# Performance work log

Measured on AMD Instinct MI355X. Metric: run time of the kernel, lower is better.

Reference implementation:

```python
import jax, jax.numpy as jnp
import numpy as np

LAYERS, BLOCKS = 10, 4
RES_CH, END_CH, CLASSES, GROUPS = 32, 256, 256, 1
BN_EPS = 1e-5


def conv1x1(x, w, b):
    # x: (bn, Cin, L), w: (Cout, Cin), b: (Cout,)
    return jnp.einsum('oc,bcl->bol', w, x) + b[None, :, None]


def mish(x):
    return x * jnp.tanh(jax.nn.softplus(x))


def concat_mish(x):
    return mish(jnp.concatenate((x, -x), axis=1))


def channel_shuffle(x, groups):
    if groups == 1:
        return x
    bn, c, l = x.shape
    return x.reshape(bn, groups, c // groups, l).transpose(0, 2, 1, 3).reshape(bn, c, l)


def batchnorm_train(x, g, b):
    # BatchNorm1d in training mode: per-channel stats over (batch, length), biased var
    m = jnp.mean(x, axis=(0, 2), keepdims=True)
    v = jnp.mean((x - m) ** 2, axis=(0, 2), keepdims=True)
    return (x - m) * jax.lax.rsqrt(v + BN_EPS) * g[None, :, None] + b[None, :, None]


def dilate(x, dilation, init_dilation, pad_start=True):
    bn, c, l = x.shape
    if dilation == 1:
        x = jnp.transpose(x, (1, 2, 0)).reshape(c, l * init_dilation, bn // init_dilation)
        return jnp.transpose(x, (2, 0, 1))
    f = dilation // init_dilation
    if f == 1:
        return x
    new_l = (l + f - 1) // f * f
    if new_l != l:
        pad = (new_l - l, 0) if pad_start else (0, new_l - l)
        x = jnp.pad(x, ((0, 0), (0, 0), pad))
        l = new_l
    l //= f
    bn *= f
    x = jnp.transpose(x, (1, 2, 0)).reshape(c, l, bn)
    return jnp.transpose(x, (2, 0, 1))


def setup_inputs() -> dict:
    key = jax.random.key(0)
    ks = iter(jax.random.split(key, 32))
    nl = LAYERS * BLOCKS
    f32 = jnp.float32
    inp = {
        'x': jax.random.normal(next(ks), (8, CLASSES, 8192), dtype=f32),
        'start_w': jax.random.normal(next(ks), (RES_CH, CLASSES), dtype=f32) * 0.05,
        'start_b': jnp.zeros((RES_CH,), f32),
        'gate_w': jax.random.normal(next(ks), (nl, RES_CH // 2, RES_CH), dtype=f32) * 0.15,
        'gate_b': jnp.zeros((nl, RES_CH // 2), f32),
        'res_w': jax.random.normal(next(ks), (nl, RES_CH, RES_CH), dtype=f32) * 0.15,
        'res_b': jnp.zeros((nl, RES_CH), f32),
        'bn_g': jnp.ones((nl, RES_CH), f32),
        'bn_b': jnp.zeros((nl, RES_CH), f32),
        'end_bn1_g': jnp.ones((RES_CH,), f32),
        'end_bn1_b': jnp.zeros((RES_CH,), f32),
        'end_conv1_w': jax.random.normal(next(ks), (END_CH // 2, 2 * RES_CH), dtype=f32) * 0.1,
        'end_conv1_b': jnp.zeros((END_CH // 2,), f32),
        'end_bn2_g': jnp.ones((END_CH // 2,), f32),
        'end_bn2_b': jnp.zeros((END_CH // 2,), f32),
        'end_conv2_w': jax.random.normal(next(ks), (CLASSES, END_CH), dtype=f32) * 0.05,
        'end_conv2_b': jnp.zeros((CLASSES,), f32),
    }
    return inp


def reference(x, start_w, start_b, gate_w, gate_b, res_w, res_b, bn_g, bn_b,
              end_bn1_g, end_bn1_b, end_conv1_w, end_conv1_b,
              end_bn2_g, end_bn2_b, end_conv2_w, end_conv2_b):
    x = conv1x1(x, start_w, start_b)
    prev_dilation = 1
    i = 0
    for block in range(BLOCKS):
        for layer in range(LAYERS):
            x = dilate(x, 2 ** layer, prev_dilation)
            prev_dilation = 2 ** layer
            x0 = x
            h = concat_mish(conv1x1(x, gate_w[i], gate_b[i]))
            h = channel_shuffle(h, GROUPS)
            h = batchnorm_train(conv1x1(h, res_w[i], res_b[i]), bn_g[i], bn_b[i])
            h = channel_shuffle(h, GROUPS)
            x = x0 + h
            i += 1
    x = concat_mish(batchnorm_train(x, end_bn1_g, end_bn1_b))
    x = concat_mish(batchnorm_train(conv1x1(x, end_conv1_w, end_conv1_b), end_bn2_g, end_bn2_b))
    x = conv1x1(x, end_conv2_w, end_conv2_b)
    x = dilate(x, 1, 2 ** (LAYERS - 1))
    return x
```

## Files before the change

kernel.cpp:

```cpp
#include <hip/hip_runtime.h>

#define BS 256
#define BSP 512
#define NBLKP 128
#define NBLK 256
#define STATS_F   0
#define W2T_F     46080
#define XBUF_F    131072
#define RBUF_F    2228224
#define WS_NEED_BYTES (4325376ull * 4ull)
#define CNTS_U  4096

__device__ __forceinline__ void mish2(float v, float& mp, float& mn) {
  float vc = fminf(fmaxf(v, -30.f), 30.f);
  float u  = __expf(vc);
  float n1 = u * (u + 2.f);
  mp = v * n1 * __builtin_amdgcn_rcpf(n1 + 2.f);
  float n2 = fmaf(2.f, u, 1.f);
  float d2 = fmaf(2.f * u, u, n2);
  mn = -v * n2 * __builtin_amdgcn_rcpf(d2);
}

__device__ __forceinline__ float coherent_ld(const float* p) {
  return __hip_atomic_load(p, __ATOMIC_RELAXED, __HIP_MEMORY_SCOPE_AGENT);
}
__device__ __forceinline__ void coherent_st(float* p, float v) {
  __hip_atomic_store(p, v, __ATOMIC_RELAXED, __HIP_MEMORY_SCOPE_AGENT);
}

template<int NT>
__device__ __forceinline__ void block_reduce_stats(const float (&vals)[32],
    float* s_red, float* s_p2, float* slot, int t) {
  #pragma unroll
  for (int cc = 0; cc < 8; ++cc) {
    float4 v = make_float4(vals[cc*4+0], vals[cc*4+1], vals[cc*4+2], vals[cc*4+3]);
    *(float4*)(&s_red[t*32 + ((cc ^ (t & 7)) << 2)]) = v;
  }
  __syncthreads();
  {
    int q = t & 63, grp = t >> 6, c = q & 31;
    bool issq = (q >= 32);
    float acc = 0.f;
    #pragma clang loop unroll_count(8)
    for (int rr = 0; rr < 64; ++rr) {
      int row = grp * 64 + rr;
      float v = s_red[row*32 + ((((c >> 2) ^ (row & 7)) << 2) | (c & 3))];
      acc = fmaf(v, issq ? v : 1.f, acc);
    }
    s_p2[t] = acc;
  }
  __syncthreads();
  if (t < 64) {
    float tot = 0.f;
    #pragma unroll
    for (int g = 0; g < NT/64; ++g) tot += s_p2[t + g*64];
    unsafeAtomicAdd(&slot[(blockIdx.x & 15) * 64 + t], tot);
  }
  __syncthreads();
}

__device__ __forceinline__ void bn32_from_slot(const float* slot, const float* g,
    const float* b, float* sA, float* sB, float* s_tmp, int t) {
  if (t < 64) {
    float s = 0.f;
    #pragma unroll
    for (int rep = 0; rep < 16; ++rep) s += slot[rep*64 + t];
    s_tmp[t] = s;
  }
  __syncthreads();
  if (t < 32) {
    float mean = s_tmp[t] * (1.f/65536.f);
    float var  = fmaf(-mean, mean, s_tmp[t+32] * (1.f/65536.f));
    float sc   = g[t] * rsqrtf(var + 1e-5f);
    sA[t] = sc;
    sB[t] = fmaf(-mean, sc, b[t]);
  }
  __syncthreads();
}

__device__ __forceinline__ void bn32_slot_coh(const float* slot, const float* g,
    const float* b, float* sA, float* sB, float* s_tmp, int t) {
  if (t < 64) {
    float s = 0.f;
    #pragma unroll
    for (int rep = 0; rep < 16; ++rep) s += coherent_ld(&slot[rep*64 + t]);
    s_tmp[t] = s;
  }
  __syncthreads();
  if (t < 32) {
    float mean = s_tmp[t] * (1.f/65536.f);
    float var  = fmaf(-mean, mean, s_tmp[t+32] * (1.f/65536.f));
    float sc   = g[t] * rsqrtf(var + 1e-5f);
    sA[t] = sc;
    sB[t] = fmaf(-mean, sc, b[t]);
  }
  __syncthreads();
}

__device__ __forceinline__ void layer_convs(const float (&x)[32], float (&r)[32],
    const float* gw, const float* gb, const float* rw, const float* rb, int i) {
  float g[16];
  #pragma unroll
  for (int j = 0; j < 16; ++j) g[j] = gb[i*16 + j];
  #pragma unroll
  for (int j = 0; j < 16; ++j)
    #pragma unroll
    for (int k = 0; k < 32; ++k)
      g[j] = fmaf(gw[i*512 + j*32 + k], x[k], g[j]);
  float cm[32];
  #pragma unroll
  for (int j = 0; j < 16; ++j) mish2(g[j], cm[j], cm[j+16]);
  #pragma unroll
  for (int j = 0; j < 32; ++j) r[j] = rb[i*32 + j];
  #pragma unroll
  for (int j = 0; j < 32; ++j)
    #pragma unroll
    for (int k = 0; k < 32; ++k)
      r[j] = fmaf(rw[i*1024 + j*32 + k], cm[k], r[j]);
}

__device__ __forceinline__ void grid_sync_lean(float* base, unsigned gen) {
  __syncthreads();
  unsigned* cnts = (unsigned*)base + CNTS_U;
  if (threadIdx.x == 0) {
    __hip_atomic_fetch_add(&cnts[(blockIdx.x & 31) * 16], 1u,
                           __ATOMIC_RELAXED, __HIP_MEMORY_SCOPE_AGENT);
    unsigned sum;
    do {
      __builtin_amdgcn_s_sleep(1);
      sum = 0;
      #pragma unroll
      for (int x = 0; x < 32; ++x)
        sum += __hip_atomic_load(&cnts[x*16], __ATOMIC_RELAXED, __HIP_MEMORY_SCOPE_AGENT);
    } while (sum < gen * NBLKP);
  }
  __syncthreads();
}

__device__ __forceinline__ void grid_sync_p(float* base, unsigned gen, bool flush) {
  __syncthreads();
  unsigned* flags = (unsigned*)base;
  unsigned* cnts  = (unsigned*)base + CNTS_U;
  if (blockIdx.x == 0) {
    if (threadIdx.x == 0) {
      if (flush) __threadfence();
      __hip_atomic_fetch_add(&cnts[0], 1u, __ATOMIC_RELAXED, __HIP_MEMORY_SCOPE_AGENT);
      unsigned sum;
      do {
        __builtin_amdgcn_s_sleep(2);
        sum = 0;
        #pragma unroll
        for (int x = 0; x < 32; ++x)
          sum += __hip_atomic_load(&cnts[x*16], __ATOMIC_RELAXED, __HIP_MEMORY_SCOPE_AGENT);
      } while (sum < gen * NBLK);
    }
    __syncthreads();
    __hip_atomic_store(&flags[threadIdx.x * 16], gen,
                       __ATOMIC_RELAXED, __HIP_MEMORY_SCOPE_AGENT);
  } else {
    if (threadIdx.x == 0) {
      if (flush) __threadfence();
      __hip_atomic_fetch_add(&cnts[(blockIdx.x & 31) * 16], 1u,
                             __ATOMIC_RELAXED, __HIP_MEMORY_SCOPE_AGENT);
      while (__hip_atomic_load(&flags[blockIdx.x * 16],
                               __ATOMIC_RELAXED, __HIP_MEMORY_SCOPE_AGENT) < gen)
        __builtin_amdgcn_s_sleep(2);
    }
    __syncthreads();
  }
}

extern "C" __global__ void __launch_bounds__(BSP, 1)
qnet_p(const float* __restrict__ xin, const float* __restrict__ sw,
       const float* __restrict__ sb, const float* __restrict__ gw,
       const float* __restrict__ gb, const float* __restrict__ rw,
       const float* __restrict__ rb, const float* __restrict__ bng,
       const float* __restrict__ bnb, const float* __restrict__ e1g,
       const float* __restrict__ e1b, const float* __restrict__ c1w,
       const float* __restrict__ c1b, const float* __restrict__ c2w,
       float* __restrict__ ws)
{
  __shared__ float s_red[BSP*32];
  __shared__ float s_p2[BSP];
  __shared__ float s_A[32], s_B[32], s_tmp[64];
  const int t = threadIdx.x, p = blockIdx.x * BSP + t;
  float* stats = ws + STATS_F;
  float* w2t   = ws + W2T_F;
  float* xb    = ws + XBUF_F;
  float* syncb = ws + RBUF_F;
  unsigned gen = 0;
  { int o = p & 255, kk = p >> 8; w2t[kk*256 + o] = c2w[o*256 + kk]; }
  const int bb = p >> 13, ll = p & 8191;
  const int pbase = bb * 2097152 + ll;
  float x[32];
  #pragma unroll
  for (int j = 0; j < 32; ++j) x[j] = sb[j];
  #pragma clang loop unroll(disable)
  for (int c8 = 0; c8 < 32; ++c8) {
    float xv[8];
    #pragma unroll
    for (int cc = 0; cc < 8; ++cc) xv[cc] = xin[pbase + (c8*8+cc)*8192];
    #pragma unroll
    for (int j = 0; j < 32; ++j)
      #pragma unroll
      for (int cc = 0; cc < 8; ++cc)
        x[j] = fmaf(sw[j*256 + c8*8 + cc], xv[cc], x[j]);
  }
  float r[32];
  layer_convs(x, r, gw, gb, rw, rb, 0);
  block_reduce_stats<BSP>(r, s_red, s_p2, stats + 0, t);
  ++gen; grid_sync_lean(syncb, gen);
  #pragma clang loop unroll(disable)
  for (int i = 1; i < 40; ++i) {
    bn32_slot_coh(stats + (i-1)*1024, bng + (i-1)*32, bnb + (i-1)*32, s_A, s_B, s_tmp, t);
    #pragma unroll
    for (int c = 0; c < 32; ++c) x[c] += fmaf(r[c], s_A[c], s_B[c]);
    layer_convs(x, r, gw, gb, rw, rb, i);
    block_reduce_stats<BSP>(r, s_red, s_p2, stats + i*1024, t);
    ++gen; grid_sync_lean(syncb, gen);
  }
  bn32_slot_coh(stats + 39*1024, bng + 39*32, bnb + 39*32, s_A, s_B, s_tmp, t);
  #pragma unroll
  for (int c = 0; c < 32; ++c) {
    x[c] += fmaf(r[c], s_A[c], s_B[c]);
    xb[c*65536 + p] = x[c];
  }
  block_reduce_stats<BSP>(x, s_red, s_p2, stats + 40*1024, t);
  ++gen; grid_sync_lean(syncb, gen);
  bn32_slot_coh(stats + 40*1024, e1g, e1b, s_A, s_B, s_tmp, t);
  float mp[32], mn[32];
  #pragma unroll
  for (int c = 0; c < 32; ++c) {
    float xh = fmaf(x[c], s_A[c], s_B[c]);
    mish2(xh, mp[c], mn[c]);
  }
  #pragma clang loop unroll(disable)
  for (int pp = 0; pp < 4; ++pp) {
    float zc[32];
    #pragma unroll
    for (int j = 0; j < 32; ++j) zc[j] = c1b[pp*32 + j];
    #pragma unroll
    for (int j = 0; j < 32; ++j)
      #pragma unroll
      for (int k = 0; k < 32; ++k) {
        zc[j] = fmaf(c1w[(pp*32+j)*64 + k],      mp[k], zc[j]);
        zc[j] = fmaf(c1w[(pp*32+j)*64 + 32 + k], mn[k], zc[j]);
      }
    block_reduce_stats<BSP>(zc, s_red, s_p2, stats + (41+pp)*1024, t);
  }
}

__global__ void __launch_bounds__(BS, 2) k_end3(const float* __restrict__ e1g,
    const float* __restrict__ e1b, const float* __restrict__ c1w,
    const float* __restrict__ c1b, const float* __restrict__ e2g,
    const float* __restrict__ e2b, const float* __restrict__ c2b,
    float* __restrict__ out, float* __restrict__ ws) {
  __shared__ float s_A[32], s_B[32], s_tmp[64];
  __shared__ float s_A2[128], s_B2[128];
  __shared__ float s_ck[2048];
  __shared__ float4 wbuf4[512];
  __shared__ float s_c1b[128];
  __shared__ float s_c2b[32];
  int t = threadIdx.x;
  const int pA = blockIdx.x * 512 + t;
  const int pB = pA + 256;
  float* stats = ws + STATS_F; float* xb = ws + XBUF_F;
  const float* w2t = ws + W2T_F;
  const int ocb = blockIdx.y * 32;
  if (t < 32) ((float4*)s_c1b)[t] = ((const float4*)c1b)[t];
  else if (t < 40) ((float4*)s_c2b)[t-32] = ((const float4*)(c2b + ocb))[t-32];
  bn32_from_slot(stats + 40*1024, e1g, e1b, s_A, s_B, s_tmp, t);
  if (t < 128) {
    int pp = t >> 5, c = t & 31;
    const float* sl = stats + (41+pp)*1024;
    float S = 0.f, Q = 0.f;
    #pragma unroll
    for (int rep = 0; rep < 16; ++rep) { S += sl[rep*64 + c]; Q += sl[rep*64 + 32 + c]; }
    float mean = S * (1.f/65536.f);
    float var  = fmaf(-mean, mean, Q * (1.f/65536.f));
    float sc   = e2g[t] * rsqrtf(var + 1e-5f);
    s_A2[t] = sc;
    s_B2[t] = fmaf(-mean, sc, e2b[t]);
  }
  __syncthreads();
  float mpA[32], mnA[32], mpB[32], mnB[32];
  #pragma unroll
  for (int c = 0; c < 32; ++c) {
    float xhA = fmaf(xb[c*65536 + pA], s_A[c], s_B[c]);
    mish2(xhA, mpA[c], mnA[c]);
    float xhB = fmaf(xb[c*65536 + pB], s_A[c], s_B[c]);
    mish2(xhB, mpB[c], mnB[c]);
  }
  float acc[64];
  #pragma unroll
  for (int o = 0; o < 32; ++o) { acc[o] = s_c2b[o]; acc[32+o] = s_c2b[o]; }
  #pragma clang loop unroll(disable)
  for (int kc = 0; kc < 4; ++kc) {
    __syncthreads();
    { const float4* cs = (const float4*)(c1w + kc*2048);
      ((float4*)s_ck)[t]       = cs[t];
      ((float4*)s_ck)[256 + t] = cs[256 + t]; }
    #pragma unroll
    for (int q = 0; q < 2; ++q) {
      int f = q*256 + t;
      int r = f >> 3, o4 = f & 7;
      int kglob = (r < 32) ? (kc*32 + r) : (96 + kc*32 + r);
      wbuf4[f] = *((const float4*)(w2t + kglob*256 + ocb) + o4);
    }
    __syncthreads();
    #pragma clang loop unroll_count(2)
    for (int j = 0; j < 32; ++j) {
      const int k = kc*32 + j;
      float zA = s_c1b[k], zB = s_c1b[k];
      const float4* cw = (const float4*)&s_ck[j*64];
      #pragma unroll
      for (int k4 = 0; k4 < 8; ++k4) {
        float4 a = cw[k4], b = cw[8+k4];
        zA = fmaf(a.x, mpA[k4*4+0], zA);
        zA = fmaf(a.y, mpA[k4*4+1], zA);
        zA = fmaf(a.z, mpA[k4*4+2], zA);
        zA = fmaf(a.w, mpA[k4*4+3], zA);
        zA = fmaf(b.x, mnA[k4*4+0], zA);
        zA = fmaf(b.y, mnA[k4*4+1], zA);
        zA = fmaf(b.z, mnA[k4*4+2], zA);
        zA = fmaf(b.w, mnA[k4*4+3], zA);
        zB = fmaf(a.x, mpB[k4*4+0], zB);
        zB = fmaf(a.y, mpB[k4*4+1], zB);
        zB = fmaf(a.z, mpB[k4*4+2], zB);
        zB = fmaf(a.w, mpB[k4*4+3], zB);
        zB = fmaf(b.x, mnB[k4*4+0], zB);
        zB = fmaf(b.y, mnB[k4*4+1], zB);
        zB = fmaf(b.z, mnB[k4*4+2], zB);
        zB = fmaf(b.w, mnB[k4*4+3], zB);
      }
      float zhA = fmaf(zA, s_A2[k], s_B2[k]);
      float mpvA, mnvA; mish2(zhA, mpvA, mnvA);
      float zhB = fmaf(zB, s_A2[k], s_B2[k]);
      float mpvB, mnvB; mish2(zhB, mpvB, mnvB);
      const float4* w0 = &wbuf4[j*8];
      const float4* w1 = &wbuf4[(32 + j)*8];
      #pragma unroll
      for (int o4 = 0; o4 < 8; ++o4) {
        float4 a = w0[o4], b = w1[o4];
        acc[o4*4+0] = fmaf(a.x, mpvA, fmaf(b.x, mnvA, acc[o4*4+0]));
        acc[o4*4+1] = fmaf(a.y, mpvA, fmaf(b.y, mnvA, acc[o4*4+1]));
        acc[o4*4+2] = fmaf(a.z, mpvA, fmaf(b.z, mnvA, acc[o4*4+2]));
        acc[o4*4+3] = fmaf(a.w, mpvA, fmaf(b.w, mnvA, acc[o4*4+3]));
        acc[32+o4*4+0] = fmaf(a.x, mpvB, fmaf(b.x, mnvB, acc[32+o4*4+0]));
        acc[32+o4*4+1] = fmaf(a.y, mpvB, fmaf(b.y, mnvB, acc[32+o4*4+1]));
        acc[32+o4*4+2] = fmaf(a.z, mpvB, fmaf(b.z, mnvB, acc[32+o4*4+2]));
        acc[32+o4*4+3] = fmaf(a.w, mpvB, fmaf(b.w, mnvB, acc[32+o4*4+3]));
      }
    }
  }
  {
    int bbA = pA >> 13, llA = pA & 8191;
    int obA = bbA * 2097152 + ocb * 8192 + llA;
    #pragma unroll
    for (int o = 0; o < 32; ++o) out[obA + o*8192] = acc[o];
    int bbB = pB >> 13, llB = pB & 8191;
    int obB = bbB * 2097152 + ocb * 8192 + llB;
    #pragma unroll
    for (int o = 0; o < 32; ++o) out[obB + o*8192] = acc[32+o];
  }
}

#define W2T_FB  4608
#define STATS_OUT_OFF (8u*1024u*1024u)
#define SLOT_STRIDE 16384

__device__ __forceinline__ void grid_sync_fb(float* ws, unsigned gen, bool flush) {
  grid_sync_p(ws, gen, flush);
}
__device__ __forceinline__ void brs_fb(const float (&vals)[32],
    float* s_red, float* s_p2, float* slot, int t) {
  #pragma unroll
  for (int cc = 0; cc < 8; ++cc) {
    float4 v = make_float4(vals[cc*4+0], vals[cc*4+1], vals[cc*4+2], vals[cc*4+3]);
    *(float4*)(&s_red[t*32 + ((cc ^ (t & 7)) << 2)]) = v;
  }
  __syncthreads();
  {
    int q = t & 63, grp = t >> 6, c = q & 31;
    bool issq = (q >= 32);
    float acc = 0.f;
    #pragma clang loop unroll_count(8)
    for (int rr = 0; rr < 64; ++rr) {
      int row = grp * 64 + rr;
      float v = s_red[row*32 + ((((c >> 2) ^ (row & 7)) << 2) | (c & 3))];
      acc = fmaf(v, issq ? v : 1.f, acc);
    }
    s_p2[t] = acc;
  }
  __syncthreads();
  if (t < 64) {
    float tot = s_p2[t] + s_p2[t+64] + s_p2[t+128] + s_p2[t+192];
    coherent_st(&slot[blockIdx.x * 64 + t], tot);
  }
}

extern "C" __global__ void __launch_bounds__(BS, 1)
qnet_fb(const float* __restrict__ xin,
        const float* __restrict__ sw, const float* __restrict__ sb,
        const float* __restrict__ gw, const float* __restrict__ gb,
        const float* __restrict__ rw, const float* __restrict__ rb,
        const float* __restrict__ bng, const float* __restrict__ bnb,
        const float* __restrict__ e1g, const float* __restrict__ e1b,
        const float* __restrict__ c1w, const float* __restrict__ c1b,
        const float* __restrict__ e2g, const float* __restrict__ e2b,
        const float* __restrict__ c2w, const float* __restrict__ c2b,
        float* __restrict__ out, float* __restrict__ ws)
{
  __shared__ float s_red[BS*32];
  __shared__ float s_p2[BS];
  __shared__ float s_tot[64];
  __shared__ float s_bcA[128];
  __shared__ float s_bcB[128];
  const int t = threadIdx.x;
  const int p = blockIdx.x * BS + t;
  float* w2t = ws + W2T_FB;
  float* zg  = out;
  float* sg  = out + STATS_OUT_OFF;
  unsigned gen = 0;
  const int bb = p >> 13, ll = p & 8191;
  const int pbase = bb * 2097152 + ll;
  { int o = p & 255, kk = p >> 8; coherent_st(&w2t[kk*256 + o], c2w[o*256 + kk]); }
  float x[32];
  #pragma unroll
  for (int j = 0; j < 32; ++j) x[j] = sb[j];
  #pragma clang loop unroll(disable)
  for (int c8 = 0; c8 < 32; ++c8) {
    float xv[8];
    #pragma unroll
    for (int cc = 0; cc < 8; ++cc) xv[cc] = xin[pbase + (c8*8+cc)*8192];
    #pragma unroll
    for (int j = 0; j < 32; ++j)
      #pragma unroll
      for (int cc = 0; cc < 8; ++cc)
        x[j] = fmaf(sw[j*256 + c8*8 + cc], xv[cc], x[j]);
  }
  #pragma clang loop unroll(disable)
  for (int i = 0; i < 40; ++i) {
    float r[32];
    layer_convs(x, r, gw, gb, rw, rb, i);
    brs_fb(r, s_red, s_p2, sg + (size_t)i * SLOT_STRIDE, t);
    ++gen; grid_sync_fb(ws, gen, false);
    {
      int q = t & 63, w = t >> 6;
      const float* col = sg + (size_t)i * SLOT_STRIDE + q;
      float acc2 = 0.f;
      #pragma clang loop unroll_count(16)
      for (int j = 0; j < 64; ++j) acc2 += coherent_ld(&col[(w*64+j)*64]);
      s_p2[t] = acc2;
    }
    __syncthreads();
    if (t < 64) s_tot[t] = s_p2[t] + s_p2[t+64] + s_p2[t+128] + s_p2[t+192];
    __syncthreads();
    if (t < 32) {
      float mean = s_tot[t] * (1.f/65536.f);
      float var  = fmaf(-mean, mean, s_tot[t+32] * (1.f/65536.f));
      float sc   = bng[i*32+t] * rsqrtf(var + 1e-5f);
      s_bcA[t] = sc;
      s_bcB[t] = fmaf(-mean, sc, bnb[i*32+t]);
    }
    __syncthreads();
    #pragma unroll
    for (int c = 0; c < 32; ++c) x[c] += fmaf(r[c], s_bcA[c], s_bcB[c]);
  }
  brs_fb(x, s_red, s_p2, sg + 40 * SLOT_STRIDE, t);
  ++gen; grid_sync_fb(ws, gen, false);
  {
    int q = t & 63, w = t >> 6;
    const float* col = sg + (size_t)40 * SLOT_STRIDE + q;
    float acc2 = 0.f;
    #pragma clang loop unroll_count(16)
    for (int j = 0; j < 64; ++j) acc2 += coherent_ld(&col[(w*64+j)*64]);
    s_p2[t] = acc2;
  }
  __syncthreads();
  if (t < 64) s_tot[t] = s_p2[t] + s_p2[t+64] + s_p2[t+128] + s_p2[t+192];
  __syncthreads();
  if (t < 32) {
    float mean = s_tot[t] * (1.f/65536.f);
    float var  = fmaf(-mean, mean, s_tot[t+32] * (1.f/65536.f));
    float sc   = e1g[t] * rsqrtf(var + 1e-5f);
    s_bcA[t] = sc;
    s_bcB[t] = fmaf(-mean, sc, e1b[t]);
  }
  __syncthreads();
  float mp[32], mn[32];
  #pragma unroll
  for (int c = 0; c < 32; ++c) {
    float xh = fmaf(x[c], s_bcA[c], s_bcB[c]);
    mish2(xh, mp[c], mn[c]);
  }
  #pragma clang loop unroll(disable)
  for (int pp = 0; pp < 4; ++pp) {
    float zc[32];
    #pragma unroll
    for (int j = 0; j < 32; ++j) zc[j] = c1b[pp*32 + j];
    #pragma unroll
    for (int j = 0; j < 32; ++j)
      #pragma unroll
      for (int k = 0; k < 32; ++k) {
        zc[j] = fmaf(c1w[(pp*32+j)*64 + k],      mp[k], zc[j]);
        zc[j] = fmaf(c1w[(pp*32+j)*64 + 32 + k], mn[k], zc[j]);
      }
    #pragma unroll
    for (int j = 0; j < 32; ++j) zg[(pp*32+j)*65536 + p] = zc[j];
    brs_fb(zc, s_red, s_p2, sg + (size_t)(41+pp) * SLOT_STRIDE, t);
    __syncthreads();
  }
  ++gen; grid_sync_fb(ws, gen, false);
  {
    int slot = 41 + (t >> 6), q = t & 63;
    const float* col = sg + (size_t)slot * SLOT_STRIDE + q;
    float acc2 = 0.f;
    #pragma clang loop unroll_count(32)
    for (int b2 = 0; b2 < 256; ++b2) acc2 += coherent_ld(&col[b2*64]);
    s_p2[t] = acc2;
  }
  __syncthreads();
  if (t < 128) {
    float S = s_p2[((t>>5)<<6) | (t&31)];
    float Q = s_p2[((t>>5)<<6) | 32 | (t&31)];
    float mean = S * (1.f/65536.f);
    float var  = fmaf(-mean, mean, Q * (1.f/65536.f));
    float sc   = e2g[t] * rsqrtf(var + 1e-5f);
    s_bcA[t] = sc;
    s_bcB[t] = fmaf(-mean, sc, e2b[t]);
  }
  __syncthreads();
  float acc[256];
  #pragma unroll
  for (int o = 0; o < 256; ++o) acc[o] = c2b[o];
  float zv_next = zg[p];
  #pragma clang loop unroll(disable)
  for (int k = 0; k < 128; ++k) {
    float zv = zv_next;
    zv_next = zg[((k+1)&127)*65536 + p];
    float zh = fmaf(zv, s_bcA[k], s_bcB[k]);
    float mpv, mnv; mish2(zh, mpv, mnv);
    const float* w0 = &w2t[k*256];
    const float* w1 = &w2t[(k+128)*256];
    #pragma unroll
    for (int o = 0; o < 256; ++o)
      acc[o] = fmaf(w0[o], mpv, fmaf(w1[o], mnv, acc[o]));
  }
  ++gen; grid_sync_fb(ws, gen, true);
  #pragma unroll
  for (int o = 0; o < 256; ++o)
    out[bb*2097152 + o*8192 + ll] = acc[o];
}

extern "C" void kernel_launch(void* const* d_in, const int* in_sizes, int n_in,
                              void* d_out, int out_size, void* d_ws, size_t ws_size,
                              hipStream_t stream) {
  const float* xin = (const float*)d_in[0];
  const float* sw  = (const float*)d_in[1];
  const float* sb  = (const float*)d_in[2];
  const float* gw  = (const float*)d_in[3];
  const float* gb  = (const float*)d_in[4];
  const float* rw  = (const float*)d_in[5];
  const float* rb  = (const float*)d_in[6];
  const float* bng = (const float*)d_in[7];
  const float* bnb = (const float*)d_in[8];
  const float* e1g = (const float*)d_in[9];
  const float* e1b = (const float*)d_in[10];
  const float* c1w = (const float*)d_in[11];
  const float* c1b = (const float*)d_in[12];
  const float* e2g = (const float*)d_in[13];
  const float* e2b = (const float*)d_in[14];
  const float* c2w = (const float*)d_in[15];
  const float* c2b = (const float*)d_in[16];
  float* out = (float*)d_out;
  float* ws  = (float*)d_ws;

  if (ws_size >= WS_NEED_BYTES) {
    hipMemsetAsync(d_ws, 0, 45 * 1024 * 4, stream);
    hipMemsetAsync((char*)d_ws + (size_t)RBUF_F * 4, 0, 4608 * 4, stream);
    void* args[] = { &xin, &sw, &sb, &gw, &gb, &rw, &rb, &bng, &bnb,
                     &e1g, &e1b, &c1w, &c1b, &c2w, &ws };
    hipError_t err = hipLaunchCooperativeKernel((const void*)qnet_p,
                                                dim3(NBLKP), dim3(BSP), args, 0, stream);
    if (err != hipSuccess) {
      hipLaunchKernelGGL(qnet_p, dim3(NBLKP), dim3(BSP), 0, stream,
                         xin, sw, sb, gw, gb, rw, rb, bng, bnb,
                         e1g, e1b, c1w, c1b, c2w, ws);
    }
    k_end3<<<dim3(128, 8), BS, 0, stream>>>(e1g, e1b, c1w, c1b, e2g, e2b, c2b, out, ws);
  } else {
    hipMemsetAsync(d_ws, 0, (CNTS_U + 512) * 4, stream);
    void* args[] = { &xin, &sw, &sb, &gw, &gb, &rw, &rb, &bng, &bnb,
                     &e1g, &e1b, &c1w, &c1b, &e2g, &e2b, &c2w, &c2b, &out, &ws };
    hipError_t err = hipLaunchCooperativeKernel((const void*)qnet_fb,
                                                dim3(NBLK), dim3(BS), args, 0, stream);
    if (err != hipSuccess) {
      hipLaunchKernelGGL(qnet_fb, dim3(NBLK), dim3(BS), 0, stream,
                         xin, sw, sb, gw, gb, rw, rb, bng, bnb,
                         e1g, e1b, c1w, c1b, e2g, e2b, c2w, c2b, out, ws);
    }
  }
}
```

Before: 1.510 ms.

## Switch persistent kernel to 256 blocks of 256 threads and simplify end kernel

The cooperative main kernel now runs 256 blocks of 256 threads instead of 128 blocks of 512. The BN stat slots are widened to 64 replicas to spread atomic contention, and the workspace offsets are moved to match. The end kernel is restructured so each thread handles one position and 64 output channels. It reads the transposed end_conv2 weights straight from global memory instead of staging them in LDS. The trade is more blocks taking part in each grid barrier and more replicas to sum on every BN read, against less per-block LDS reduction work and lower register pressure.

```diff
diff --git a/kernel.cpp b/kernel.cpp
--- a/kernel.cpp
+++ b/kernel.cpp
@@ -1,13 +1,14 @@
 #include <hip/hip_runtime.h>
 
 #define BS 256
-#define BSP 512
-#define NBLKP 128
+#define NBLKP 256
 #define NBLK 256
+#define NREP 64
+#define SLOT_F 4096
 #define STATS_F   0
-#define W2T_F     46080
-#define XBUF_F    131072
-#define RBUF_F    2228224
+#define W2T_F     184320
+#define XBUF_F    262144
+#define SYNC_F    2359296
 #define WS_NEED_BYTES (4325376ull * 4ull)
 #define CNTS_U  4096
 
@@ -28,7 +29,6 @@
   __hip_atomic_store(p, v, __ATOMIC_RELAXED, __HIP_MEMORY_SCOPE_AGENT);
 }
 
-template<int NT>
 __device__ __forceinline__ void block_reduce_stats(const float (&vals)[32],
     float* s_red, float* s_p2, float* slot, int t) {
   #pragma unroll
@@ -51,10 +51,8 @@
   }
   __syncthreads();
   if (t < 64) {
-    float tot = 0.f;
-    #pragma unroll
-    for (int g = 0; g < NT/64; ++g) tot += s_p2[t + g*64];
-    unsafeAtomicAdd(&slot[(blockIdx.x & 15) * 64 + t], tot);
+    float tot = s_p2[t] + s_p2[t+64] + s_p2[t+128] + s_p2[t+192];
+    unsafeAtomicAdd(&slot[(blockIdx.x & (NREP-1)) * 64 + t], tot);
   }
   __syncthreads();
 }
@@ -64,7 +62,7 @@
   if (t < 64) {
     float s = 0.f;
     #pragma unroll
-    for (int rep = 0; rep < 16; ++rep) s += slot[rep*64 + t];
+    for (int rep = 0; rep < NREP; ++rep) s += slot[rep*64 + t];
     s_tmp[t] = s;
   }
   __syncthreads();
@@ -83,7 +81,7 @@
   if (t < 64) {
     float s = 0.f;
     #pragma unroll
-    for (int rep = 0; rep < 16; ++rep) s += coherent_ld(&slot[rep*64 + t]);
+    for (int rep = 0; rep < NREP; ++rep) s += coherent_ld(&slot[rep*64 + t]);
     s_tmp[t] = s;
   }
   __syncthreads();
@@ -170,7 +168,7 @@
   }
 }
 
-extern "C" __global__ void __launch_bounds__(BSP, 1)
+extern "C" __global__ void __launch_bounds__(BS, 1)
 qnet_p(const float* __restrict__ xin, const float* __restrict__ sw,
        const float* __restrict__ sb, const float* __restrict__ gw,
        const float* __restrict__ gb, const float* __restrict__ rw,
@@ -180,14 +178,14 @@
        const float* __restrict__ c1b, const float* __restrict__ c2w,
        float* __restrict__ ws)
 {
-  __shared__ float s_red[BSP*32];
-  __shared__ float s_p2[BSP];
+  __shared__ float s_red[BS*32];
+  __shared__ float s_p2[BS];
   __shared__ float s_A[32], s_B[32], s_tmp[64];
-  const int t = threadIdx.x, p = blockIdx.x * BSP + t;
+  const int t = threadIdx.x, p = blockIdx.x * BS + t;
   float* stats = ws + STATS_F;
   float* w2t   = ws + W2T_F;
   float* xb    = ws + XBUF_F;
-  float* syncb = ws + RBUF_F;
+  float* syncb = ws + SYNC_F;
   unsigned gen = 0;
   { int o = p & 255, kk = p >> 8; w2t[kk*256 + o] = c2w[o*256 + kk]; }
   const int bb = p >> 13, ll = p & 8191;
@@ -208,26 +206,26 @@
   }
   float r[32];
   layer_convs(x, r, gw, gb, rw, rb, 0);
-  block_reduce_stats<BSP>(r, s_red, s_p2, stats + 0, t);
+  block_reduce_stats(r, s_red, s_p2, stats + 0, t);
   ++gen; grid_sync_lean(syncb, gen);
   #pragma clang loop unroll(disable)
   for (int i = 1; i < 40; ++i) {
-    bn32_slot_coh(stats + (i-1)*1024, bng + (i-1)*32, bnb + (i-1)*32, s_A, s_B, s_tmp, t);
+    bn32_slot_coh(stats + (i-1)*SLOT_F, bng + (i-1)*32, bnb + (i-1)*32, s_A, s_B, s_tmp, t);
     #pragma unroll
     for (int c = 0; c < 32; ++c) x[c] += fmaf(r[c], s_A[c], s_B[c]);
     layer_convs(x, r, gw, gb, rw, rb, i);
-    block_reduce_stats<BSP>(r, s_red, s_p2, stats + i*1024, t);
+    block_reduce_stats(r, s_red, s_p2, stats + i*SLOT_F, t);
     ++gen; grid_sync_lean(syncb, gen);
   }
-  bn32_slot_coh(stats + 39*1024, bng + 39*32, bnb + 39*32, s_A, s_B, s_tmp, t);
+  bn32_slot_coh(stats + 39*SLOT_F, bng + 39*32, bnb + 39*32, s_A, s_B, s_tmp, t);
   #pragma unroll
   for (int c = 0; c < 32; ++c) {
     x[c] += fmaf(r[c], s_A[c], s_B[c]);
     xb[c*65536 + p] = x[c];
   }
-  block_reduce_stats<BSP>(x, s_red, s_p2, stats + 40*1024, t);
+  block_reduce_stats(x, s_red, s_p2, stats + 40*SLOT_F, t);
   ++gen; grid_sync_lean(syncb, gen);
-  bn32_slot_coh(stats + 40*1024, e1g, e1b, s_A, s_B, s_tmp, t);
+  bn32_slot_coh(stats + 40*SLOT_F, e1g, e1b, s_A, s_B, s_tmp, t);
   float mp[32], mn[32];
   #pragma unroll
   for (int c = 0; c < 32; ++c) {
@@ -246,11 +244,11 @@
         zc[j] = fmaf(c1w[(pp*32+j)*64 + k],      mp[k], zc[j]);
         zc[j] = fmaf(c1w[(pp*32+j)*64 + 32 + k], mn[k], zc[j]);
       }
-    block_reduce_stats<BSP>(zc, s_red, s_p2, stats + (41+pp)*1024, t);
-  }
-}
-
-__global__ void __launch_bounds__(BS, 2) k_end3(const float* __restrict__ e1g,
+    block_reduce_stats(zc, s_red, s_p2, stats + (41+pp)*SLOT_F, t);
+  }
+}
+
+__global__ void __launch_bounds__(BS) k_end3(const float* __restrict__ e1g,
     const float* __restrict__ e1b, const float* __restrict__ c1w,
     const float* __restrict__ c1b, const float* __restrict__ e2g,
     const float* __restrict__ e2b, const float* __restrict__ c2b,
@@ -258,24 +256,21 @@
   __shared__ float s_A[32], s_B[32], s_tmp[64];
   __shared__ float s_A2[128], s_B2[128];
   __shared__ float s_ck[2048];
-  __shared__ float4 wbuf4[512];
   __shared__ float s_c1b[128];
-  __shared__ float s_c2b[32];
-  int t = threadIdx.x;
-  const int pA = blockIdx.x * 512 + t;
-  const int pB = pA + 256;
+  __shared__ float s_c2b[64];
+  int t = threadIdx.x, p = blockIdx.x * BS + t;
   float* stats = ws + STATS_F; float* xb = ws + XBUF_F;
   const float* w2t = ws + W2T_F;
-  const int ocb = blockIdx.y * 32;
+  const int ocb = blockIdx.y * 64;
   if (t < 32) ((float4*)s_c1b)[t] = ((const float4*)c1b)[t];
-  else if (t < 40) ((float4*)s_c2b)[t-32] = ((const float4*)(c2b + ocb))[t-32];
-  bn32_from_slot(stats + 40*1024, e1g, e1b, s_A, s_B, s_tmp, t);
+  else if (t < 48) ((float4*)s_c2b)[t-32] = ((const float4*)(c2b + ocb))[t-32];
+  bn32_from_slot(stats + 40*SLOT_F, e1g, e1b, s_A, s_B, s_tmp, t);
   if (t < 128) {
     int pp = t >> 5, c = t & 31;
-    const float* sl = stats + (41+pp)*1024;
+    const float* sl = stats + (41+pp)*SLOT_F;
     float S = 0.f, Q = 0.f;
     #pragma unroll
-    for (int rep = 0; rep < 16; ++rep) { S += sl[rep*64 + c]; Q += sl[rep*64 + 32 + c]; }
+    for (int rep = 0; rep < NREP; ++rep) { S += sl[rep*64 + c]; Q += sl[rep*64 + 32 + c]; }
     float mean = S * (1.f/65536.f);
     float var  = fmaf(-mean, mean, Q * (1.f/65536.f));
     float sc   = e2g[t] * rsqrtf(var + 1e-5f);
@@ -283,86 +278,52 @@
     s_B2[t] = fmaf(-mean, sc, e2b[t]);
   }
   __syncthreads();
-  float mpA[32], mnA[32], mpB[32], mnB[32];
+  float mp[32], mn[32];
   #pragma unroll
   for (int c = 0; c < 32; ++c) {
-    float xhA = fmaf(xb[c*65536 + pA], s_A[c], s_B[c]);
-    mish2(xhA, mpA[c], mnA[c]);
-    float xhB = fmaf(xb[c*65536 + pB], s_A[c], s_B[c]);
-    mish2(xhB, mpB[c], mnB[c]);
+    float xh = fmaf(xb[c*65536 + p], s_A[c], s_B[c]);
+    mish2(xh, mp[c], mn[c]);
   }
   float acc[64];
   #pragma unroll
-  for (int o = 0; o < 32; ++o) { acc[o] = s_c2b[o]; acc[32+o] = s_c2b[o]; }
+  for (int o = 0; o < 64; ++o) acc[o] = s_c2b[o];
   #pragma clang loop unroll(disable)
   for (int kc = 0; kc < 4; ++kc) {
     __syncthreads();
     { const float4* cs = (const float4*)(c1w + kc*2048);
       ((float4*)s_ck)[t]       = cs[t];
       ((float4*)s_ck)[256 + t] = cs[256 + t]; }
-    #pragma unroll
-    for (int q = 0; q < 2; ++q) {
-      int f = q*256 + t;
-      int r = f >> 3, o4 = f & 7;
-      int kglob = (r < 32) ? (kc*32 + r) : (96 + kc*32 + r);
-      wbuf4[f] = *((const float4*)(w2t + kglob*256 + ocb) + o4);
-    }
     __syncthreads();
     #pragma clang loop unroll_count(2)
     for (int j = 0; j < 32; ++j) {
       const int k = kc*32 + j;
-      float zA = s_c1b[k], zB = s_c1b[k];
+      float z = s_c1b[k];
       const float4* cw = (const float4*)&s_ck[j*64];
       #pragma unroll
       for (int k4 = 0; k4 < 8; ++k4) {
         float4 a = cw[k4], b = cw[8+k4];
-        zA = fmaf(a.x, mpA[k4*4+0], zA);
-        zA = fmaf(a.y, mpA[k4*4+1], zA);
-        zA = fmaf(a.z, mpA[k4*4+2], zA);
-        zA = fmaf(a.w, mpA[k4*4+3], zA);
-        zA = fmaf(b.x, mnA[k4*4+0], zA);
-        zA = fmaf(b.y, mnA[k4*4+1], zA);
-        zA = fmaf(b.z, mnA[k4*4+2], zA);
-        zA = fmaf(b.w, mnA[k4*4+3], zA);
-        zB = fmaf(a.x, mpB[k4*4+0], zB);
-        zB = fmaf(a.y, mpB[k4*4+1], zB);
-        zB = fmaf(a.z, mpB[k4*4+2], zB);
-        zB = fmaf(a.w, mpB[k4*4+3], zB);
-        zB = fmaf(b.x, mnB[k4*4+0], zB);
-        zB = fmaf(b.y, mnB[k4*4+1], zB);
-        zB = fmaf(b.z, mnB[k4*4+2], zB);
-        zB = fmaf(b.w, mnB[k4*4+3], zB);
+        z = fmaf(a.x, mp[k4*4+0], z);
+        z = fmaf(a.y, mp[k4*4+1], z);
+        z = fmaf(a.z, mp[k4*4+2], z);
+        z = fmaf(a.w, mp[k4*4+3], z);
+        z = fmaf(b.x, mn[k4*4+0], z);
+        z = fmaf(b.y, mn[k4*4+1], z);
+        z = fmaf(b.z, mn[k4*4+2], z);
+        z = fmaf(b.w, mn[k4*4+3], z);
       }
-      float zhA = fmaf(zA, s_A2[k], s_B2[k]);
-      float mpvA, mnvA; mish2(zhA, mpvA, mnvA);
-      float zhB = fmaf(zB, s_A2[k], s_B2[k]);
-      float mpvB, mnvB; mish2(zhB, mpvB, mnvB);
-      const float4* w0 = &wbuf4[j*8];
-      const float4* w1 = &wbuf4[(32 + j)*8];
-      #pragma unroll
-      for (int o4 = 0; o4 < 8; ++o4) {
-        float4 a = w0[o4], b = w1[o4];
-        acc[o4*4+0] = fmaf(a.x, mpvA, fmaf(b.x, mnvA, acc[o4*4+0]));
-        acc[o4*4+1] = fmaf(a.y, mpvA, fmaf(b.y, mnvA, acc[o4*4+1]));
-        acc[o4*4+2] = fmaf(a.z, mpvA, fmaf(b.z, mnvA, acc[o4*4+2]));
-        acc[o4*4+3] = fmaf(a.w, mpvA, fmaf(b.w, mnvA, acc[o4*4+3]));
-        acc[32+o4*4+0] = fmaf(a.x, mpvB, fmaf(b.x, mnvB, acc[32+o4*4+0]));
-        acc[32+o4*4+1] = fmaf(a.y, mpvB, fmaf(b.y, mnvB, acc[32+o4*4+1]));
-        acc[32+o4*4+2] = fmaf(a.z, mpvB, fmaf(b.z, mnvB, acc[32+o4*4+2]));
-        acc[32+o4*4+3] = fmaf(a.w, mpvB, fmaf(b.w, mnvB, acc[32+o4*4+3]));
-      }
-    }
-  }
-  {
-    int bbA = pA >> 13, llA = pA & 8191;
-    int obA = bbA * 2097152 + ocb * 8192 + llA;
-    #pragma unroll
-    for (int o = 0; o < 32; ++o) out[obA + o*8192] = acc[o];
-    int bbB = pB >> 13, llB = pB & 8191;
-    int obB = bbB * 2097152 + ocb * 8192 + llB;
-    #pragma unroll
-    for (int o = 0; o < 32; ++o) out[obB + o*8192] = acc[32+o];
-  }
+      float zh = fmaf(z, s_A2[k], s_B2[k]);
+      float mpv, mnv; mish2(zh, mpv, mnv);
+      const float* w0 = w2t + k*256 + ocb;
+      const float* w1 = w2t + (k+128)*256 + ocb;
+      #pragma unroll
+      for (int o = 0; o < 64; ++o)
+        acc[o] = fmaf(w0[o], mpv, fmaf(w1[o], mnv, acc[o]));
+    }
+  }
+  int bb = p >> 13, ll = p & 8191;
+  int obase = bb * 2097152 + ocb * 8192 + ll;
+  #pragma unroll
+  for (int o = 0; o < 64; ++o) out[obase + o*8192] = acc[o];
 }
 
 #define W2T_FB  4608
@@ -577,18 +538,18 @@
   float* ws  = (float*)d_ws;
 
   if (ws_size >= WS_NEED_BYTES) {
-    hipMemsetAsync(d_ws, 0, 45 * 1024 * 4, stream);
-    hipMemsetAsync((char*)d_ws + (size_t)RBUF_F * 4, 0, 4608 * 4, stream);
+    hipMemsetAsync(d_ws, 0, 45 * SLOT_F * 4, stream);
+    hipMemsetAsync((char*)d_ws + (size_t)SYNC_F * 4, 0, 4608 * 4, stream);
     void* args[] = { &xin, &sw, &sb, &gw, &gb, &rw, &rb, &bng, &bnb,
                      &e1g, &e1b, &c1w, &c1b, &c2w, &ws };
     hipError_t err = hipLaunchCooperativeKernel((const void*)qnet_p,
-                                                dim3(NBLKP), dim3(BSP), args, 0, stream);
+                                                dim3(NBLKP), dim3(BS), args, 0, stream);
     if (err != hipSuccess) {
-      hipLaunchKernelGGL(qnet_p, dim3(NBLKP), dim3(BSP), 0, stream,
+      hipLaunchKernelGGL(qnet_p, dim3(NBLKP), dim3(BS), 0, stream,
                          xin, sw, sb, gw, gb, rw, rb, bng, bnb,
                          e1g, e1b, c1w, c1b, c2w, ws);
     }
-    k_end3<<<dim3(128, 8), BS, 0, stream>>>(e1g, e1b, c1w, c1b, e2g, e2b, c2b, out, ws);
+    k_end3<<<dim3(256, 4), BS, 0, stream>>>(e1g, e1b, c1w, c1b, e2g, e2b, c2b, out, ws);
   } else {
     hipMemsetAsync(d_ws, 0, (CNTS_U + 512) * 4, stream);
     void* args[] = { &xin, &sw, &sb, &gw, &gb, &rw, &rb, &bng, &bnb,
```

New measurement: 1.550 ms. 1.03x slower.
